# Performance work log

Measured on AMD Instinct MI355X. Metric: run time of the kernel, lower is better.

Reference implementation:

```python
import jax, jax.numpy as jnp
import numpy as np

D_MODEL, D_HEAD, N_HEAD = 1024, 64, 16
B, T1, T2 = 2, 2048, 2048


def setup_inputs() -> dict:
    key = jax.random.key(0)
    ks = jax.random.split(key, 8)
    s = 1.0 / np.sqrt(D_MODEL)
    return {
        "x": jax.random.normal(ks[0], (B, T1, D_MODEL), dtype=jnp.float32),
        "context": jax.random.normal(ks[1], (B, T2, D_MODEL), dtype=jnp.float32),
        "bias": jax.random.normal(ks[2], (T1, T2), dtype=jnp.float32),
        "W_q": jax.random.normal(ks[3], (D_MODEL, N_HEAD * D_HEAD), dtype=jnp.float32) * s,
        "W_k": jax.random.normal(ks[4], (D_MODEL, N_HEAD * D_HEAD), dtype=jnp.float32) * s,
        "W_v": jax.random.normal(ks[5], (D_MODEL, N_HEAD * D_HEAD), dtype=jnp.float32) * s,
        "W_out": jax.random.normal(ks[6], (N_HEAD * D_HEAD, D_MODEL), dtype=jnp.float32) * s,
        "b_out": jnp.zeros((D_MODEL,), dtype=jnp.float32),
    }


def reference(x, context, bias, W_q, W_k, W_v, W_out, b_out):
    Bq, T1_, _ = x.shape
    T2_ = context.shape[1]
    atten_scale = 1.0 / np.sqrt(D_HEAD)
    # fixed (non-trainable) per-head scale: 2^{-1}, ..., 2^{-n_head}
    head_scale = jnp.exp2(-jnp.arange(1, N_HEAD + 1, dtype=jnp.float32))

    # projections -> [B, H, T, d]
    q = (x @ W_q).reshape(Bq, T1_, N_HEAD, D_HEAD).transpose(0, 2, 1, 3)
    k = (context @ W_k).reshape(Bq, T2_, N_HEAD, D_HEAD).transpose(0, 2, 1, 3)
    v = (context @ W_v).reshape(Bq, T2_, N_HEAD, D_HEAD).transpose(0, 2, 1, 3)

    # scores: [B, H, T1, T2]
    scores = jnp.einsum("bhqd,bhkd->bhqk", q, k) * atten_scale
    scores = scores + bias[None, None, :, :] * head_scale[None, :, None, None]
    attn = jax.nn.softmax(scores, axis=-1)

    out = jnp.einsum("bhqk,bhkd->bqhd", attn, v).reshape(Bq, T1_, N_HEAD * D_HEAD)
    # dropout is identity in eval mode
    return out @ W_out + b_out
```

## Files before the change

kernel.cpp:

```cpp
#include <hip/hip_runtime.h>

typedef float  f32x4   __attribute__((ext_vector_type(4)));
typedef float  f32x16  __attribute__((ext_vector_type(16)));
typedef __bf16 bf16x8  __attribute__((ext_vector_type(8)));
typedef __bf16 bf16x4  __attribute__((ext_vector_type(4)));
typedef __bf16 bf16x2  __attribute__((ext_vector_type(2)));
typedef short  short8v __attribute__((ext_vector_type(8)));
typedef unsigned uint4v __attribute__((ext_vector_type(4)));

__device__ __forceinline__ short f2bf(float f) {
  unsigned u = __float_as_uint(f);
  unsigned r = (u + 0x7FFFu + ((u >> 16) & 1u)) >> 16;
  return (short)r;
}

__device__ __forceinline__ float exp2_native(float x) {
#if __has_builtin(__builtin_amdgcn_exp2f)
  return __builtin_amdgcn_exp2f(x);
#else
  float r;
  asm("v_exp_f32 %0, %1" : "=v"(r) : "v"(x));
  return r;
#endif
}

__device__ __forceinline__ f32x4 mfma16(bf16x8 a, bf16x8 b, f32x4 c) {
  return __builtin_amdgcn_mfma_f32_16x16x32_bf16(a, b, c, 0, 0, 0);
}
__device__ __forceinline__ f32x16 mfma32(bf16x8 a, bf16x8 b, f32x16 c) {
  return __builtin_amdgcn_mfma_f32_32x32x16_bf16(a, b, c, 0, 0, 0);
}

__device__ __forceinline__ void gload16(const void* g, void* l) {
  __builtin_amdgcn_global_load_lds(
      (const __attribute__((address_space(1))) unsigned int*)g,
      (__attribute__((address_space(3))) unsigned int*)l,
      16, 0, 0);
}

__device__ __forceinline__ bf16x8 p_exchange(const unsigned* pk, int a, int hi) {
  unsigned y1 = hi ? pk[4 * a + 0] : pk[4 * a + 2];
  unsigned z1 = __shfl_xor(y1, 32);
  unsigned y2 = hi ? pk[4 * a + 1] : pk[4 * a + 3];
  unsigned z2 = __shfl_xor(y2, 32);
  unsigned w0 = hi ? z1 : pk[4 * a + 0];
  unsigned w1 = hi ? z2 : pk[4 * a + 1];
  unsigned w2 = hi ? pk[4 * a + 2] : z1;
  unsigned w3 = hi ? pk[4 * a + 3] : z2;
  uint4v q4 = {w0, w1, w2, w3};
  return __builtin_bit_cast(bf16x8, q4);
}


__global__ __launch_bounds__(256) void cvt_copy(const float* __restrict__ in,
                                                short* __restrict__ out, int n4) {
  int i = blockIdx.x * blockDim.x + threadIdx.x;
  int stride = gridDim.x * blockDim.x;
  for (; i < n4; i += stride) {
    float4 v = *(const float4*)&in[i * 4];
    short4 o;
    o.x = f2bf(v.x); o.y = f2bf(v.y); o.z = f2bf(v.z); o.w = f2bf(v.w);
    *(short4*)&out[i * 4] = o;
  }
}

__global__ __launch_bounds__(256) void cvt_transpose4(const float* __restrict__ W0,
                                                      const float* __restrict__ W1,
                                                      const float* __restrict__ W2,
                                                      const float* __restrict__ W3,
                                                      short* __restrict__ T0,
                                                      short* __restrict__ T1,
                                                      short* __restrict__ T2,
                                                      short* __restrict__ T3) {
  __shared__ short t_s[64][72];
  int z = blockIdx.z;
  const float* W = (z == 0) ? W0 : (z == 1) ? W1 : (z == 2) ? W2 : W3;
  short* Wt = (z == 0) ? T0 : (z == 1) ? T1 : (z == 2) ? T2 : T3;
  int k0 = blockIdx.y * 64, n0 = blockIdx.x * 64;
  int tid = threadIdx.x;
#pragma unroll
  for (int i = 0; i < 4; i++) {
    int idx = i * 256 + tid;
    int r = idx >> 4, cg = idx & 15;
    float4 v = *(const float4*)&W[(k0 + r) * 1024 + n0 + cg * 4];
    t_s[cg * 4 + 0][r] = f2bf(v.x);
    t_s[cg * 4 + 1][r] = f2bf(v.y);
    t_s[cg * 4 + 2][r] = f2bf(v.z);
    t_s[cg * 4 + 3][r] = f2bf(v.w);
  }
  __syncthreads();
#pragma unroll
  for (int i = 0; i < 2; i++) {
    int idx = i * 256 + tid;
    int r = idx >> 3, cg = idx & 7;
    short8v val = *(short8v*)&t_s[r][cg * 8];
    *(short8v*)&Wt[(n0 + r) * 1024 + k0 + cg * 8] = val;
  }
}

template <int EPI>
__global__ __launch_bounds__(256, 4) void gemm_bf16(const short* __restrict__ A,
                                                    const short* __restrict__ Bt,
                                                    void* __restrict__ out,
                                                    void* __restrict__ out2,
                                                    const float* __restrict__ bout) {
  constexpr int KD = 1024;
  constexpr int NB = (EPI == 3) ? 32 : 16;
  __shared__ short a_s[64][64];
  __shared__ short b_s[64][64];
  int tid = threadIdx.x, w = tid >> 6, lane = tid & 63;
  int g = lane >> 4, c16 = lane & 15;
  int hsw = c16 & 7;

  int lin = blockIdx.x + NB * blockIdx.y;
  int wk = (lin & 7) * (NB * 8) + (lin >> 3);
  int c0 = (wk & (NB - 1)) * 64, r0 = (wk / NB) * 64;

  int wr = (w >> 1) * 32, wc = (w & 1) * 32;
  f32x4 acc[2][2] = {};

  for (int kt = 0; kt < KD / 64; ++kt) {
    int k0 = kt * 64;
    __syncthreads();
#pragma unroll
    for (int i = 0; i < 2; i++) {
      int cb = i * 256 + w * 64;
      int c = cb + lane;
      int row = c >> 3, kg = c & 7;
      int sw = (kg ^ (row & 7)) * 8;
      gload16(A + (r0 + row) * KD + k0 + sw, (char*)a_s + cb * 16);
      gload16(Bt + (c0 + row) * KD + k0 + sw, (char*)b_s + cb * 16);
    }
    __syncthreads();
#pragma unroll
    for (int kk = 0; kk < 2; kk++) {
      bf16x8 af[2], bf[2];
      int sl0 = ((4 * kk + g) ^ hsw) * 8;
#pragma unroll
      for (int m = 0; m < 2; m++) af[m] = *(const bf16x8*)&a_s[wr + m * 16 + c16][sl0];
#pragma unroll
      for (int n = 0; n < 2; n++) bf[n] = *(const bf16x8*)&b_s[wc + n * 16 + c16][sl0];
#pragma unroll
      for (int m = 0; m < 2; m++)
#pragma unroll
        for (int n = 0; n < 2; n++) acc[m][n] = mfma16(af[m], bf[n], acc[m][n]);
    }
  }

#pragma unroll
  for (int m = 0; m < 2; m++)
#pragma unroll
    for (int n = 0; n < 2; n++)
#pragma unroll
      for (int r = 0; r < 4; r++) {
        int row = r0 + wr + m * 16 + g * 4 + r;
        int col = c0 + wc + n * 16 + c16;
        float v = acc[m][n][r];
        int b = row >> 11, t = row & 2047;
        if (EPI == 2) {
          ((float*)out)[row * 1024 + col] = v + bout[col];
        } else if (EPI == 0) {
          int h = col >> 6, d = col & 63;
          ((short*)out)[(((b * 16 + h) * 2048) + t) * 64 + d] = f2bf(v);
        } else {
          if (col < 1024) {
            int h = col >> 6, d = col & 63;
            ((short*)out)[(((b * 16 + h) * 2048) + t) * 64 + d] = f2bf(v);
          } else {
            int cv = col - 1024;
            int h = cv >> 6, d = cv & 63;
            ((short*)out2)[(((b * 16 + h) * 64) + d) * 2048 + t] = f2bf(v);
          }
        }
      }
}

__global__ __launch_bounds__(512, 4) void flash_attn(const short* __restrict__ Qg,
                                                     const short* __restrict__ Kg,
                                                     const short* __restrict__ Vtg,
                                                     const short* __restrict__ biasb,
                                                     short* __restrict__ Og) {
  __shared__ short k_s[2][2][64][64];
  __shared__ short v_s[2][2][64][64];

  int tid = threadIdx.x, w = tid >> 6, lane = tid & 63;
  int gid = w >> 2, w4 = w & 3;
  int hi = lane >> 5, ll = lane & 31, l7 = ll & 7;

  int lin = blockIdx.x + 16 * (blockIdx.y + 16 * blockIdx.z);
  int wk = (lin & 7) * 64 + (lin >> 3);
  int qb = (wk & 15) * 128;
  int h = (wk >> 4) & 15;
  int b = wk >> 8;

  const short* Qh = Qg + (size_t)(b * 16 + h) * 2048 * 64;
  const short* Kh = Kg + (size_t)(b * 16 + h) * 2048 * 64;
  const short* Vh = Vtg + (size_t)(b * 16 + h) * 64 * 2048;

  const float C1 = 0.125f * 1.44269504f;
  const float C2 = exp2f(-(float)(h + 1)) * 1.44269504f;

  int qrow = qb + w4 * 32 + ll;
  const short* bp = biasb + (size_t)qrow * 2048 + 4 * hi;

  int srow = tid >> 3, st8 = tid & 7;
  int ssw = (st8 ^ (srow & 7)) * 8;

  {
    gload16(Kh + srow * 64 + ssw, (char*)&k_s[0][0][0][0] + w * 64 * 16);
    gload16(Vh + srow * 2048 + ssw, (char*)&v_s[0][0][0][0] + w * 64 * 16);
    gload16(Kh + 64 * 64 + srow * 64 + ssw, (char*)&k_s[0][1][0][0] + w * 64 * 16);
    gload16(Vh + srow * 2048 + 64 + ssw, (char*)&v_s[0][1][0][0] + w * 64 * 16);
  }
  bf16x4 bvA0[4], bvA1[4];
#pragma unroll
  for (int u = 0; u < 4; u++) {
    bvA0[u] = *(const bf16x4*)(bp + gid * 64 + u * 8);
    bvA1[u] = *(const bf16x4*)(bp + gid * 64 + 32 + u * 8);
  }
  bf16x8 qf[4];
#pragma unroll
  for (int dm = 0; dm < 4; dm++)
    qf[dm] = *(const bf16x8*)(Qh + (size_t)qrow * 64 + dm * 16 + hi * 8);
  asm volatile("" ::: "memory");

  float l0 = 0.f, l1 = 0.f, l2 = 0.f, l3 = 0.f;
  f32x16 o_acc[2] = {};

  for (int r = 0; r < 16; ++r) {
    int cur = r & 1;
    int kt = 2 * r + gid;

    bf16x4 bvB0[4], bvB1[4];
    if (r < 15) {
      const short* bpn = bp + (kt + 2) * 64;
#pragma unroll
      for (int u = 0; u < 4; u++) {
        bvB0[u] = *(const bf16x4*)(bpn + u * 8);
        bvB1[u] = *(const bf16x4*)(bpn + 32 + u * 8);
      }
      int tA = 2 * r + 2;
      gload16(Kh + (size_t)tA * 4096 + srow * 64 + ssw,
              (char*)&k_s[cur ^ 1][0][0][0] + w * 64 * 16);
      gload16(Vh + srow * 2048 + tA * 64 + ssw,
              (char*)&v_s[cur ^ 1][0][0][0] + w * 64 * 16);
      gload16(Kh + (size_t)(tA + 1) * 4096 + srow * 64 + ssw,
              (char*)&k_s[cur ^ 1][1][0][0] + w * 64 * 16);
      gload16(Vh + srow * 2048 + (tA + 1) * 64 + ssw,
              (char*)&v_s[cur ^ 1][1][0][0] + w * 64 * 16);
      asm volatile("s_waitcnt vmcnt(12)" ::: "memory");
    } else {
      asm volatile("s_waitcnt vmcnt(0)" ::: "memory");
    }
    __builtin_amdgcn_s_barrier();

    f32x16 sacc = {};
    __builtin_amdgcn_s_setprio(1);
#pragma unroll
    for (int dm = 0; dm < 4; dm++) {
      const short* kr = &k_s[cur][gid][ll][((2 * dm + hi) ^ l7) * 8];
      sacc = mfma32(*(const bf16x8*)kr, qf[dm], sacc);
    }
    __builtin_amdgcn_s_setprio(0);

    unsigned pk[8];
#pragma unroll
    for (int i = 0; i < 8; i++) {
      float b0 = (float)bvA0[i >> 1][2 * (i & 1)];
      float b1 = (float)bvA0[i >> 1][2 * (i & 1) + 1];
      float p0 = exp2_native(sacc[2 * i] * C1 + b0 * C2);
      float p1 = exp2_native(sacc[2 * i + 1] * C1 + b1 * C2);
      l0 += p0; l1 += p1;
      bf16x2 pp = {(__bf16)p0, (__bf16)p1};
      pk[i] = __builtin_bit_cast(unsigned, pp);
    }

    __builtin_amdgcn_s_setprio(1);
#pragma unroll
    for (int a = 0; a < 2; a++) {
      bf16x8 PA = p_exchange(pk, a, hi);
#pragma unroll
      for (int dt = 0; dt < 2; dt++) {
        const short* vr = &v_s[cur][gid][dt * 32 + ll][((2 * a + hi) ^ l7) * 8];
        o_acc[dt] = mfma32(PA, *(const bf16x8*)vr, o_acc[dt]);
      }
    }
    __builtin_amdgcn_s_setprio(0);
    asm volatile("" ::: "memory");

    f32x16 sacc1 = {};
    __builtin_amdgcn_s_setprio(1);
#pragma unroll
    for (int dm = 0; dm < 4; dm++) {
      const short* kr = &k_s[cur][gid][32 + ll][((2 * dm + hi) ^ l7) * 8];
      sacc1 = mfma32(*(const bf16x8*)kr, qf[dm], sacc1);
    }
    __builtin_amdgcn_s_setprio(0);

#pragma unroll
    for (int i = 0; i < 8; i++) {
      float b0 = (float)bvA1[i >> 1][2 * (i & 1)];
      float b1 = (float)bvA1[i >> 1][2 * (i & 1) + 1];
      float p0 = exp2_native(sacc1[2 * i] * C1 + b0 * C2);
      float p1 = exp2_native(sacc1[2 * i + 1] * C1 + b1 * C2);
      l2 += p0; l3 += p1;
      bf16x2 pp = {(__bf16)p0, (__bf16)p1};
      pk[i] = __builtin_bit_cast(unsigned, pp);
    }

    __builtin_amdgcn_s_setprio(1);
#pragma unroll
    for (int a = 0; a < 2; a++) {
      bf16x8 PA = p_exchange(pk, a, hi);
#pragma unroll
      for (int dt = 0; dt < 2; dt++) {
        const short* vr = &v_s[cur][gid][dt * 32 + ll][((4 + 2 * a + hi) ^ l7) * 8];
        o_acc[dt] = mfma32(PA, *(const bf16x8*)vr, o_acc[dt]);
      }
    }
    __builtin_amdgcn_s_setprio(0);
    __builtin_amdgcn_s_barrier();

#pragma unroll
    for (int u = 0; u < 4; u++) { bvA0[u] = bvB0[u]; bvA1[u] = bvB1[u]; }
  }

  float l_run = (l0 + l1) + (l2 + l3);

  l_run += __shfl_xor(l_run, 32);
  float* ox = (float*)&k_s[0][0][0][0];
  float* lx = (float*)&v_s[0][0][0][0];
  if (gid == 1) {
#pragma unroll
    for (int k = 0; k < 32; k++)
      ox[(w4 * 32 + k) * 64 + lane] = o_acc[k >> 4][k & 15];
    if (lane < 32) lx[w4 * 32 + lane] = l_run;
  }
  __syncthreads();
  if (gid == 0) {
    float invl = 1.f / (l_run + lx[w4 * 32 + ll]);
#pragma unroll
    for (int k = 0; k < 32; k++)
      o_acc[k >> 4][k & 15] += ox[(w4 * 32 + k) * 64 + lane];

#pragma unroll
    for (int r = 0; r < 16; r++) {
      int q = (r & 3) + 8 * (r >> 2) + 4 * hi;
      float iv = __shfl(invl, q);
      int tg = qb + w4 * 32 + q;
#pragma unroll
      for (int dt = 0; dt < 2; dt++) {
        Og[(size_t)(b * 2048 + tg) * 1024 + h * 64 + dt * 32 + ll] =
            f2bf(o_acc[dt][r] * iv);
      }
    }
  }
}

extern "C" void kernel_launch(void* const* d_in, const int* in_sizes, int n_in,
                              void* d_out, int out_size, void* d_ws, size_t ws_size,
                              hipStream_t stream) {
  const float* x    = (const float*)d_in[0];
  const float* ctx  = (const float*)d_in[1];
  const float* bias = (const float*)d_in[2];
  const float* Wq   = (const float*)d_in[3];
  const float* Wk   = (const float*)d_in[4];
  const float* Wv   = (const float*)d_in[5];
  const float* Wo   = (const float*)d_in[6];
  const float* bo   = (const float*)d_in[7];
  float* out = (float*)d_out;

  char* ws = (char*)d_ws;
  short* x_bf = (short*)(ws + 0);
  short* c_bf = (short*)(ws + 8388608);
  short* wq_t = (short*)(ws + 16777216);
  short* wk_t = (short*)(ws + 18874368);
  short* wv_t = (short*)(ws + 20971520);
  short* wo_t = (short*)(ws + 23068672);
  short* q_ws = (short*)(ws + 25165824);
  short* k_ws = (short*)(ws + 33554432);
  short* v_ws = (short*)(ws + 41943040);
  short* o_ws = (short*)(ws + 50331648);
  short* bias_bf = x_bf;

  cvt_copy<<<1024, 256, 0, stream>>>(x, x_bf, 1048576);
  cvt_copy<<<1024, 256, 0, stream>>>(ctx, c_bf, 1048576);
  dim3 tg(16, 16, 4);
  cvt_transpose4<<<tg, 256, 0, stream>>>(Wq, Wk, Wv, Wo, wq_t, wk_t, wv_t, wo_t);

  dim3 gq(16, 64);
  gemm_bf16<0><<<gq, 256, 0, stream>>>(x_bf, wq_t, q_ws, nullptr, nullptr);
  dim3 gkv(32, 64);
  gemm_bf16<3><<<gkv, 256, 0, stream>>>(c_bf, wk_t, k_ws, v_ws, nullptr);

  cvt_copy<<<1024, 256, 0, stream>>>(bias, bias_bf, 1048576);

  dim3 fg(16, 16, 2);
  flash_attn<<<fg, 512, 0, stream>>>(q_ws, k_ws, v_ws, bias_bf, o_ws);

  gemm_bf16<2><<<gq, 256, 0, stream>>>(o_ws, wo_t, out, nullptr, bo);
}
```

Measured before the change: 176.9 us.

## Pre-swizzle bias into MFMA fragment layout and drop setprio hints

Replaces the plain bias fp32-to-bf16 conversion with a kernel that writes the bias already arranged in the per-lane MFMA accumulator fragment order. Each lane of the attention kernel can then fetch its bias values with four fully coalesced 16-byte loads per tile instead of eight strided 8-byte loads, and the vmcnt wait is adjusted to match. It also removes the s_setprio calls around the MFMA sections. The conversion kernel is more complex, but its cost is similar to the plain copy it replaces.

```diff
diff --git a/kernel.cpp b/kernel.cpp
--- a/kernel.cpp
+++ b/kernel.cpp
@@ -3,7 +3,6 @@
 typedef float  f32x4   __attribute__((ext_vector_type(4)));
 typedef float  f32x16  __attribute__((ext_vector_type(16)));
 typedef __bf16 bf16x8  __attribute__((ext_vector_type(8)));
-typedef __bf16 bf16x4  __attribute__((ext_vector_type(4)));
 typedef __bf16 bf16x2  __attribute__((ext_vector_type(2)));
 typedef short  short8v __attribute__((ext_vector_type(8)));
 typedef unsigned uint4v __attribute__((ext_vector_type(4)));
@@ -62,6 +61,31 @@
     o.x = f2bf(v.x); o.y = f2bf(v.y); o.z = f2bf(v.z); o.w = f2bf(v.w);
     *(short4*)&out[i * 4] = o;
   }
+}
+
+__global__ __launch_bounds__(256) void cvt_bias_frag(const float* __restrict__ bias,
+                                                     short* __restrict__ frag) {
+  __shared__ short lb[2][2][64][8];
+  int kt = blockIdx.x, w4 = blockIdx.y, Qi = blockIdx.z;
+  int t = threadIdx.x;
+  int row = t >> 3;
+  int c0 = (t & 7) * 8;
+  const float* src = bias + (size_t)(Qi * 128 + w4 * 32 + row) * 2048 + kt * 64 + c0;
+  float4 v0 = *(const float4*)(src + 0);
+  float4 v1 = *(const float4*)(src + 4);
+  float vv[8] = {v0.x, v0.y, v0.z, v0.w, v1.x, v1.y, v1.z, v1.w};
+#pragma unroll
+  for (int j = 0; j < 8; j++) {
+    int kc64 = c0 + j;
+    int s = kc64 >> 5, kc5 = kc64 & 31;
+    int hi = (kc5 >> 2) & 1, a = kc5 & 3, bq = kc5 >> 3;
+    int half = bq >> 1, idx = a + 4 * (bq & 1);
+    lb[s][half][hi * 32 + row][idx] = f2bf(vv[j]);
+  }
+  __syncthreads();
+  short8v val = ((const short8v*)&lb[0][0][0][0])[t];
+  size_t base = ((size_t)((Qi * 4 + w4) * 32 + kt)) * 2048;
+  *(short8v*)&frag[base + t * 8] = val;
 }
 
 __global__ __launch_bounds__(256) void cvt_transpose4(const float* __restrict__ W0,
@@ -178,7 +202,7 @@
 __global__ __launch_bounds__(512, 4) void flash_attn(const short* __restrict__ Qg,
                                                      const short* __restrict__ Kg,
                                                      const short* __restrict__ Vtg,
-                                                     const short* __restrict__ biasb,
+                                                     const short* __restrict__ bfrag,
                                                      short* __restrict__ Og) {
   __shared__ short k_s[2][2][64][64];
   __shared__ short v_s[2][2][64][64];
@@ -189,7 +213,8 @@
 
   int lin = blockIdx.x + 16 * (blockIdx.y + 16 * blockIdx.z);
   int wk = (lin & 7) * 64 + (lin >> 3);
-  int qb = (wk & 15) * 128;
+  int Qi = wk & 15;
+  int qb = Qi * 128;
   int h = (wk >> 4) & 15;
   int b = wk >> 8;
 
@@ -201,7 +226,7 @@
   const float C2 = exp2f(-(float)(h + 1)) * 1.44269504f;
 
   int qrow = qb + w4 * 32 + ll;
-  const short* bp = biasb + (size_t)qrow * 2048 + 4 * hi;
+  const short* bw = bfrag + ((size_t)(Qi * 4 + w4) * 32) * 2048 + lane * 8;
 
   int srow = tid >> 3, st8 = tid & 7;
   int ssw = (st8 ^ (srow & 7)) * 8;
@@ -212,12 +237,10 @@
     gload16(Kh + 64 * 64 + srow * 64 + ssw, (char*)&k_s[0][1][0][0] + w * 64 * 16);
     gload16(Vh + srow * 2048 + 64 + ssw, (char*)&v_s[0][1][0][0] + w * 64 * 16);
   }
-  bf16x4 bvA0[4], bvA1[4];
-#pragma unroll
-  for (int u = 0; u < 4; u++) {
-    bvA0[u] = *(const bf16x4*)(bp + gid * 64 + u * 8);
-    bvA1[u] = *(const bf16x4*)(bp + gid * 64 + 32 + u * 8);
-  }
+  bf16x8 bvA[4];
+#pragma unroll
+  for (int j = 0; j < 4; j++)
+    bvA[j] = *(const bf16x8*)(bw + (size_t)gid * 2048 + j * 512);
   bf16x8 qf[4];
 #pragma unroll
   for (int dm = 0; dm < 4; dm++)
@@ -231,14 +254,11 @@
     int cur = r & 1;
     int kt = 2 * r + gid;
 
-    bf16x4 bvB0[4], bvB1[4];
+    bf16x8 bvB[4];
     if (r < 15) {
-      const short* bpn = bp + (kt + 2) * 64;
-#pragma unroll
-      for (int u = 0; u < 4; u++) {
-        bvB0[u] = *(const bf16x4*)(bpn + u * 8);
-        bvB1[u] = *(const bf16x4*)(bpn + 32 + u * 8);
-      }
+#pragma unroll
+      for (int j = 0; j < 4; j++)
+        bvB[j] = *(const bf16x8*)(bw + (size_t)(kt + 2) * 2048 + j * 512);
       int tA = 2 * r + 2;
       gload16(Kh + (size_t)tA * 4096 + srow * 64 + ssw,
               (char*)&k_s[cur ^ 1][0][0][0] + w * 64 * 16);
@@ -248,26 +268,24 @@
               (char*)&k_s[cur ^ 1][1][0][0] + w * 64 * 16);
       gload16(Vh + srow * 2048 + (tA + 1) * 64 + ssw,
               (char*)&v_s[cur ^ 1][1][0][0] + w * 64 * 16);
-      asm volatile("s_waitcnt vmcnt(12)" ::: "memory");
+      asm volatile("s_waitcnt vmcnt(8)" ::: "memory");
     } else {
       asm volatile("s_waitcnt vmcnt(0)" ::: "memory");
     }
     __builtin_amdgcn_s_barrier();
 
     f32x16 sacc = {};
-    __builtin_amdgcn_s_setprio(1);
 #pragma unroll
     for (int dm = 0; dm < 4; dm++) {
       const short* kr = &k_s[cur][gid][ll][((2 * dm + hi) ^ l7) * 8];
       sacc = mfma32(*(const bf16x8*)kr, qf[dm], sacc);
     }
-    __builtin_amdgcn_s_setprio(0);
 
     unsigned pk[8];
 #pragma unroll
     for (int i = 0; i < 8; i++) {
-      float b0 = (float)bvA0[i >> 1][2 * (i & 1)];
-      float b1 = (float)bvA0[i >> 1][2 * (i & 1) + 1];
+      float b0 = (float)(i < 4 ? bvA[0][2 * i] : bvA[1][2 * i - 8]);
+      float b1 = (float)(i < 4 ? bvA[0][2 * i + 1] : bvA[1][2 * i - 7]);
       float p0 = exp2_native(sacc[2 * i] * C1 + b0 * C2);
       float p1 = exp2_native(sacc[2 * i + 1] * C1 + b1 * C2);
       l0 += p0; l1 += p1;
@@ -275,7 +293,6 @@
       pk[i] = __builtin_bit_cast(unsigned, pp);
     }
 
-    __builtin_amdgcn_s_setprio(1);
 #pragma unroll
     for (int a = 0; a < 2; a++) {
       bf16x8 PA = p_exchange(pk, a, hi);
@@ -285,22 +302,19 @@
         o_acc[dt] = mfma32(PA, *(const bf16x8*)vr, o_acc[dt]);
       }
     }
-    __builtin_amdgcn_s_setprio(0);
     asm volatile("" ::: "memory");
 
     f32x16 sacc1 = {};
-    __builtin_amdgcn_s_setprio(1);
 #pragma unroll
     for (int dm = 0; dm < 4; dm++) {
       const short* kr = &k_s[cur][gid][32 + ll][((2 * dm + hi) ^ l7) * 8];
       sacc1 = mfma32(*(const bf16x8*)kr, qf[dm], sacc1);
     }
-    __builtin_amdgcn_s_setprio(0);
 
 #pragma unroll
     for (int i = 0; i < 8; i++) {
-      float b0 = (float)bvA1[i >> 1][2 * (i & 1)];
-      float b1 = (float)bvA1[i >> 1][2 * (i & 1) + 1];
+      float b0 = (float)(i < 4 ? bvA[2][2 * i] : bvA[3][2 * i - 8]);
+      float b1 = (float)(i < 4 ? bvA[2][2 * i + 1] : bvA[3][2 * i - 7]);
       float p0 = exp2_native(sacc1[2 * i] * C1 + b0 * C2);
       float p1 = exp2_native(sacc1[2 * i + 1] * C1 + b1 * C2);
       l2 += p0; l3 += p1;
@@ -308,7 +322,6 @@
       pk[i] = __builtin_bit_cast(unsigned, pp);
     }
 
-    __builtin_amdgcn_s_setprio(1);
 #pragma unroll
     for (int a = 0; a < 2; a++) {
       bf16x8 PA = p_exchange(pk, a, hi);
@@ -318,11 +331,10 @@
         o_acc[dt] = mfma32(PA, *(const bf16x8*)vr, o_acc[dt]);
       }
     }
-    __builtin_amdgcn_s_setprio(0);
     __builtin_amdgcn_s_barrier();
 
 #pragma unroll
-    for (int u = 0; u < 4; u++) { bvA0[u] = bvB0[u]; bvA1[u] = bvB1[u]; }
+    for (int j = 0; j < 4; j++) bvA[j] = bvB[j];
   }
 
   float l_run = (l0 + l1) + (l2 + l3);
@@ -381,7 +393,7 @@
   short* k_ws = (short*)(ws + 33554432);
   short* v_ws = (short*)(ws + 41943040);
   short* o_ws = (short*)(ws + 50331648);
-  short* bias_bf = x_bf;
+  short* bias_fr = x_bf;
 
   cvt_copy<<<1024, 256, 0, stream>>>(x, x_bf, 1048576);
   cvt_copy<<<1024, 256, 0, stream>>>(ctx, c_bf, 1048576);
@@ -393,10 +405,11 @@
   dim3 gkv(32, 64);
   gemm_bf16<3><<<gkv, 256, 0, stream>>>(c_bf, wk_t, k_ws, v_ws, nullptr);
 
-  cvt_copy<<<1024, 256, 0, stream>>>(bias, bias_bf, 1048576);
+  dim3 bg(32, 4, 16);
+  cvt_bias_frag<<<bg, 256, 0, stream>>>(bias, bias_fr);
 
   dim3 fg(16, 16, 2);
-  flash_attn<<<fg, 512, 0, stream>>>(q_ws, k_ws, v_ws, bias_bf, o_ws);
+  flash_attn<<<fg, 512, 0, stream>>>(q_ws, k_ws, v_ws, bias_fr, o_ws);
 
   gemm_bf16<2><<<gq, 256, 0, stream>>>(o_ws, wo_t, out, nullptr, bo);
 }
```

New measurement: 174.3 us. Within noise of the previous version (-1.5%).
